# Kernel tuning notes

Measured on AMD Instinct MI355X. Metric: run time of the kernel, lower is better.

Reference implementation:

```python
import jax, jax.numpy as jnp
import numpy as np

UNITS = 512

def _lstm_scan(x_tbf, W, U, b):
    # x_tbf: [T, B, F]; W: [F, 4U]; U: [U, 4U]; b: [4U]
    B = x_tbf.shape[1]
    h0 = jnp.zeros((B, UNITS), dtype=x_tbf.dtype)
    c0 = jnp.zeros((B, UNITS), dtype=x_tbf.dtype)

    def step(carry, x_t):
        h, c = carry
        z = x_t @ W + h @ U + b  # [B, 4U], Keras gate order i,f,g,o
        i, f, g, o = jnp.split(z, 4, axis=-1)
        i = jax.nn.sigmoid(i)
        f = jax.nn.sigmoid(f)
        g = jnp.tanh(g)
        o = jax.nn.sigmoid(o)
        c = f * c + i * g
        h = o * jnp.tanh(c)
        return (h, c), None

    (h, c), _ = jax.lax.scan(step, (h0, c0), x_tbf)
    return h, c


def setup_inputs() -> dict:
    key = jax.random.key(0)
    ks = jax.random.split(key, 7)
    B, T, F = 32, 2048, 256
    s_in = 1.0 / np.sqrt(F)
    s_rec = 1.0 / np.sqrt(UNITS)
    return {
        "inputs": jax.random.normal(ks[0], (B, T, F), dtype=jnp.float32),
        "W_f": jax.random.normal(ks[1], (F, 4 * UNITS), dtype=jnp.float32) * s_in,
        "U_f": jax.random.normal(ks[2], (UNITS, 4 * UNITS), dtype=jnp.float32) * s_rec,
        "b_f": jax.random.normal(ks[3], (4 * UNITS,), dtype=jnp.float32) * 0.01,
        "W_b": jax.random.normal(ks[4], (F, 4 * UNITS), dtype=jnp.float32) * s_in,
        "U_b": jax.random.normal(ks[5], (UNITS, 4 * UNITS), dtype=jnp.float32) * s_rec,
        "b_b": jax.random.normal(ks[6], (4 * UNITS,), dtype=jnp.float32) * 0.01,
    }


def reference(inputs, W_f, U_f, b_f, W_b, U_b, b_b):
    # inputs: [B, T, F] -> scan over time: [T, B, F]
    x = jnp.swapaxes(inputs, 0, 1)
    h_f, c_f = _lstm_scan(x, W_f, U_f, b_f)              # forward direction
    h_b, c_b = _lstm_scan(x[::-1], W_b, U_b, b_b)        # backward: reversed time
    merged = jnp.concatenate([h_f, h_b], axis=-1)        # [B, 2*UNITS]
    return (merged, h_f, c_f, h_b, c_b)
```

## Files before the change

### kernel.cpp

```cpp
#include <hip/hip_runtime.h>

#define T_STEPS 2048
#define NWG 64

typedef __bf16 bf16x8 __attribute__((ext_vector_type(8)));
typedef float f32x4 __attribute__((ext_vector_type(4)));
typedef unsigned long long u64;

#define XBF_OFF   0ull
#define FLAGS_OFF 33554432ull
#define HBUF_OFF  (FLAGS_OFF + 4096ull)
#define WS_NEEDED (HBUF_OFF + 131072ull)

__device__ __forceinline__ unsigned short f2bf(float f) {
    unsigned int u = __builtin_bit_cast(unsigned int, f);
    u = u + 0x7fffu + ((u >> 16) & 1u);
    return (unsigned short)(u >> 16);
}
__device__ __forceinline__ float sigf(float x) { return 1.0f / (1.0f + __expf(-x)); }
__device__ __forceinline__ float tanhfast(float x) { return 1.0f - 2.0f / (__expf(2.0f * x) + 1.0f); }

__global__ void prep_x(const float* __restrict__ X, unsigned short* __restrict__ Xbf) {
    unsigned int idx = blockIdx.x * 256u + threadIdx.x;
    unsigned int k4 = idx & 63u;
    unsigned int b  = (idx >> 6) & 31u;
    unsigned int t  = idx >> 11;
    float4 v = *(const float4*)(X + ((size_t)b * 2048u + t) * 256u + k4 * 4u);
    u64 pk = (u64)f2bf(v.x)
           | ((u64)f2bf(v.y) << 16)
           | ((u64)f2bf(v.z) << 32)
           | ((u64)f2bf(v.w) << 48);
    *(u64*)(Xbf + ((size_t)t * 32u + b) * 256u + k4 * 4u) = pk;
}

__global__ __launch_bounds__(256, 1) void lstm_rec(
    const unsigned short* __restrict__ Xbf,
    const float* __restrict__ W_f, const float* __restrict__ U_f, const float* __restrict__ b_f,
    const float* __restrict__ W_b, const float* __restrict__ U_b, const float* __restrict__ b_b,
    float* __restrict__ out, unsigned int* flags, unsigned int* Hbuf)
{
    const int wg = blockIdx.x;
    const int d  = wg >> 5;
    const int s  = wg & 31;
    const int c0 = s * 16;
    const int tid = threadIdx.x;

    const float* Wm = d ? W_b : W_f;
    const float* Um = d ? U_b : U_f;
    const float* bia = d ? b_b : b_f;

    __shared__ __align__(16) unsigned char s_u[65536];
    __shared__ __align__(16) unsigned char s_w[32768];
    __shared__ __align__(16) unsigned char s_h[32768];
    __shared__ __align__(16) unsigned char s_x[16384];
    __shared__ float s_S[32][64];
    __shared__ float s_bias[64];
    __shared__ int s_abort;

    {
        int cl = tid & 15, g = (tid >> 4) & 3, k0 = tid >> 6;
        int n = g * 16 + cl;
        int gcol = g * 512 + c0 + cl;
        for (int i = 0; i < 128; ++i) {
            int k = k0 + i * 4;
            unsigned short v = f2bf(Um[(size_t)k * 2048 + gcol]);
            unsigned int addr = (unsigned)(n * 1024 + k * 2) ^ (unsigned)((n & 7) << 4);
            *(unsigned short*)(s_u + addr) = v;
        }
        for (int i = 0; i < 64; ++i) {
            int k = k0 + i * 4;
            unsigned short v = f2bf(Wm[(size_t)k * 2048 + gcol]);
            unsigned int addr = (unsigned)(n * 512 + k * 2) ^ (unsigned)((n & 7) << 4);
            *(unsigned short*)(s_w + addr) = v;
        }
        if (tid < 64) s_bias[tid] = bia[(tid >> 4) * 512 + c0 + (tid & 15)];
        if (tid == 0) s_abort = 0;
        for (int i = 0; i < 16; ++i)
            *(u64*)(s_h + (tid + i * 256) * 8) = 0ull;
        int t_x = d ? (T_STEPS - 1) : 0;
        const u64* xsrc = (const u64*)(Xbf + (size_t)t_x * 32 * 256);
        for (int i = 0; i < 8; ++i) {
            int ch = tid + i * 256;
            int b = ch >> 6;
            unsigned int addr = (unsigned)(ch * 8) ^ (unsigned)((b & 7) << 4);
            *(u64*)(s_x + addr) = xsrc[ch];
        }
    }
    __syncthreads();

    const int g  = tid >> 6;
    const int l  = tid & 63;
    const int cl = l & 15;
    const int h4 = l >> 4;
    const int n  = g * 16 + cl;
    const unsigned int uO = (unsigned)(n * 1024 + h4 * 16);
    const unsigned int wO = (unsigned)(n * 512  + h4 * 16);
    const unsigned int nS = (unsigned)((n & 7) << 4);
    const int b0 = cl, b1 = cl + 16;
    const unsigned int hO0 = (unsigned)(b0 * 1024 + h4 * 16);
    const unsigned int hO1 = (unsigned)(b1 * 1024 + h4 * 16);
    const unsigned int xO0 = (unsigned)(b0 * 512  + h4 * 16);
    const unsigned int xO1 = (unsigned)(b1 * 512  + h4 * 16);
    const unsigned int bS0 = (unsigned)((b0 & 7) << 4);
    const unsigned int bS1 = (unsigned)((b1 & 7) << 4);

    const unsigned int fBase  = (unsigned)(d * 32);
    const unsigned int myFlag = fBase + (unsigned)s;
    const unsigned int pollA  = fBase + (unsigned)(l & 15);
    const unsigned int pollB  = fBase + 16u + (unsigned)(l & 15);

    const int eb  = tid >> 3;
    const int ecp = (tid & 7) * 2;
    float c_reg[2] = {0.f, 0.f};

    bf16x8 wBr[8];
    #pragma unroll
    for (int kc = 0; kc < 8; ++kc)
        wBr[kc] = *(const bf16x8*)(s_w + ((wO + kc * 64) ^ nS));
    bf16x8 uBr[16];
    #pragma unroll
    for (int kc = 0; kc < 16; ++kc)
        uBr[kc] = *(const bf16x8*)(s_u + ((uO + kc * 64) ^ nS));

    f32x4 axc0 = {0.f, 0.f, 0.f, 0.f};
    f32x4 axc1 = {0.f, 0.f, 0.f, 0.f};
    #pragma unroll
    for (int kc = 0; kc < 8; ++kc) {
        bf16x8 a0 = *(const bf16x8*)(s_x + ((xO0 + kc * 64) ^ bS0));
        bf16x8 a1 = *(const bf16x8*)(s_x + ((xO1 + kc * 64) ^ bS1));
        axc0 = __builtin_amdgcn_mfma_f32_16x16x32_bf16(a0, wBr[kc], axc0, 0, 0, 0);
        axc1 = __builtin_amdgcn_mfma_f32_16x16x32_bf16(a1, wBr[kc], axc1, 0, 0, 0);
    }

    for (int t = 0; t < T_STEPS; ++t) {
        f32x4 acc0 = axc0;
        f32x4 acc1 = axc1;

        if (t > 0) {
            u64* hsrc = (u64*)Hbuf + (size_t)(d * 2 + (t & 1)) * 4096;

            {
                unsigned int spin = 0;
                for (;;) {
                    unsigned int v = __hip_atomic_load(&flags[pollA], __ATOMIC_RELAXED, __HIP_MEMORY_SCOPE_AGENT);
                    if (__all((int)(v >= (unsigned)t))) break;
                    if (++spin > (1u << 21)) { s_abort = 1; break; }
                    if (spin > 64) __builtin_amdgcn_s_sleep(1);
                }
            }
            u64 ra[8];
            #pragma unroll
            for (int i = 0; i < 8; ++i) {
                int idx = tid + i * 256;
                ra[i] = __hip_atomic_load(&hsrc[(idx >> 6) * 128 + (idx & 63)], __ATOMIC_RELAXED, __HIP_MEMORY_SCOPE_AGENT);
            }
            {
                unsigned int spin = 0;
                for (;;) {
                    unsigned int v = __hip_atomic_load(&flags[pollB], __ATOMIC_RELAXED, __HIP_MEMORY_SCOPE_AGENT);
                    if (__all((int)(v >= (unsigned)t))) break;
                    if (++spin > (1u << 21)) { s_abort = 1; break; }
                    if (spin > 64) __builtin_amdgcn_s_sleep(1);
                }
            }
            u64 rb[8];
            #pragma unroll
            for (int i = 0; i < 8; ++i) {
                int idx = tid + i * 256;
                rb[i] = __hip_atomic_load(&hsrc[(idx >> 6) * 128 + 64 + (idx & 63)], __ATOMIC_RELAXED, __HIP_MEMORY_SCOPE_AGENT);
            }
            #pragma unroll
            for (int i = 0; i < 8; ++i) {
                int idx = tid + i * 256;
                int b = idx >> 6;
                unsigned int addr = (unsigned)(b * 1024 + (idx & 63) * 8) ^ (unsigned)((b & 7) << 4);
                *(u64*)(s_h + addr) = ra[i];
            }
            __syncthreads();
            #pragma unroll
            for (int kc = 0; kc < 8; ++kc) {
                bf16x8 a0 = *(const bf16x8*)(s_h + ((hO0 + kc * 64) ^ bS0));
                bf16x8 a1 = *(const bf16x8*)(s_h + ((hO1 + kc * 64) ^ bS1));
                acc0 = __builtin_amdgcn_mfma_f32_16x16x32_bf16(a0, uBr[kc], acc0, 0, 0, 0);
                acc1 = __builtin_amdgcn_mfma_f32_16x16x32_bf16(a1, uBr[kc], acc1, 0, 0, 0);
            }
            #pragma unroll
            for (int i = 0; i < 8; ++i) {
                int idx = tid + i * 256;
                int b = idx >> 6;
                unsigned int addr = (unsigned)(b * 1024 + 512 + (idx & 63) * 8) ^ (unsigned)((b & 7) << 4);
                *(u64*)(s_h + addr) = rb[i];
            }
            __syncthreads();
            #pragma unroll
            for (int kc = 8; kc < 16; ++kc) {
                bf16x8 a0 = *(const bf16x8*)(s_h + ((hO0 + kc * 64) ^ bS0));
                bf16x8 a1 = *(const bf16x8*)(s_h + ((hO1 + kc * 64) ^ bS1));
                acc0 = __builtin_amdgcn_mfma_f32_16x16x32_bf16(a0, uBr[kc], acc0, 0, 0, 0);
                acc1 = __builtin_amdgcn_mfma_f32_16x16x32_bf16(a1, uBr[kc], acc1, 0, 0, 0);
            }
        }

        #pragma unroll
        for (int r = 0; r < 4; ++r) {
            s_S[h4 * 4 + r][n]      = acc0[r];
            s_S[16 + h4 * 4 + r][n] = acc1[r];
        }
        __syncthreads();
        if (s_abort) return;

        float hv[2];
        #pragma unroll
        for (int j = 0; j < 2; ++j) {
            int cx = ecp + j;
            float zi = s_S[eb][cx]      + s_bias[cx];
            float zf = s_S[eb][16 + cx] + s_bias[16 + cx];
            float zg = s_S[eb][32 + cx] + s_bias[32 + cx];
            float zo = s_S[eb][48 + cx] + s_bias[48 + cx];
            float ii = sigf(zi), ff = sigf(zf), gg = tanhfast(zg), oo = sigf(zo);
            float c = ff * c_reg[j] + ii * gg;
            c_reg[j] = c;
            hv[j] = oo * tanhfast(c);
        }

        if (t == T_STEPS - 1) {
            #pragma unroll
            for (int j = 0; j < 2; ++j) {
                int col = c0 + ecp + j;
                out[(size_t)eb * 1024 + d * 512 + col] = hv[j];
                out[32768 + d * 32768 + (size_t)eb * 512 + col] = hv[j];
                out[49152 + d * 32768 + (size_t)eb * 512 + col] = c_reg[j];
            }
            break;
        }

        const int nb = (t + 1) & 1;
        unsigned int hp = (unsigned)f2bf(hv[0]) | ((unsigned)f2bf(hv[1]) << 16);
        unsigned int hidx = (unsigned)((d * 2 + nb) * 8192 + eb * 256 + ((c0 + ecp) >> 1));
        __hip_atomic_store(&Hbuf[hidx], hp, __ATOMIC_RELAXED, __HIP_MEMORY_SCOPE_AGENT);

        __syncthreads();
        if (tid == 0)
            __hip_atomic_store(&flags[myFlag], (unsigned)(t + 1), __ATOMIC_RELAXED, __HIP_MEMORY_SCOPE_AGENT);

        {
            int t_x = d ? (T_STEPS - 2 - t) : (t + 1);
            const u64* xsrc = (const u64*)(Xbf + (size_t)t_x * 32 * 256);
            #pragma unroll
            for (int i = 0; i < 8; ++i) {
                int ch = tid + i * 256;
                int b = ch >> 6;
                unsigned int addr = (unsigned)(ch * 8) ^ (unsigned)((b & 7) << 4);
                *(u64*)(s_x + addr) = xsrc[ch];
            }
        }
        __syncthreads();
        axc0 = f32x4{0.f, 0.f, 0.f, 0.f};
        axc1 = f32x4{0.f, 0.f, 0.f, 0.f};
        #pragma unroll
        for (int kc = 0; kc < 8; ++kc) {
            bf16x8 a0 = *(const bf16x8*)(s_x + ((xO0 + kc * 64) ^ bS0));
            bf16x8 a1 = *(const bf16x8*)(s_x + ((xO1 + kc * 64) ^ bS1));
            axc0 = __builtin_amdgcn_mfma_f32_16x16x32_bf16(a0, wBr[kc], axc0, 0, 0, 0);
            axc1 = __builtin_amdgcn_mfma_f32_16x16x32_bf16(a1, wBr[kc], axc1, 0, 0, 0);
        }
    }
}

extern "C" void kernel_launch(void* const* d_in, const int* in_sizes, int n_in,
                              void* d_out, int out_size, void* d_ws, size_t ws_size,
                              hipStream_t stream) {
    if (ws_size < WS_NEEDED) return;

    const float* X   = (const float*)d_in[0];
    const float* W_f = (const float*)d_in[1];
    const float* U_f = (const float*)d_in[2];
    const float* b_f = (const float*)d_in[3];
    const float* W_b = (const float*)d_in[4];
    const float* U_b = (const float*)d_in[5];
    const float* b_b = (const float*)d_in[6];

    unsigned short* Xbf  = (unsigned short*)d_ws;
    unsigned int*  flags = (unsigned int*)((char*)d_ws + FLAGS_OFF);
    unsigned int*  Hbuf  = (unsigned int*)((char*)d_ws + HBUF_OFF);

    hipMemsetAsync(flags, 0, 4096, stream);
    prep_x<<<16384, 256, 0, stream>>>(X, Xbf);

    float* out = (float*)d_out;
    void* args[] = {(void*)&Xbf, (void*)&W_f, (void*)&U_f, (void*)&b_f,
                    (void*)&W_b, (void*)&U_b, (void*)&b_b,
                    (void*)&out, (void*)&flags, (void*)&Hbuf};
    hipLaunchCooperativeKernel((void*)lstm_rec, dim3(NWG), dim3(256), args, 0, stream);
}
```

Baseline: 6.461 ms.

## Split batch across 8 groups of workgroups and use XCC-local plain loads when co-located

```diff
diff --git a/kernel.cpp b/kernel.cpp
--- a/kernel.cpp
+++ b/kernel.cpp
@@ -1,7 +1,7 @@
 #include <hip/hip_runtime.h>
 
 #define T_STEPS 2048
-#define NWG 64
+#define NWG 256
 
 typedef __bf16 bf16x8 __attribute__((ext_vector_type(8)));
 typedef float f32x4 __attribute__((ext_vector_type(4)));
@@ -9,7 +9,8 @@
 
 #define XBF_OFF   0ull
 #define FLAGS_OFF 33554432ull
-#define HBUF_OFF  (FLAGS_OFF + 4096ull)
+#define XSLOT_OFF (FLAGS_OFF + 1024ull)
+#define HBUF_OFF  (XSLOT_OFF + 1024ull)
 #define WS_NEEDED (HBUF_OFF + 131072ull)
 
 __device__ __forceinline__ unsigned short f2bf(float f) {
@@ -37,12 +38,14 @@
     const unsigned short* __restrict__ Xbf,
     const float* __restrict__ W_f, const float* __restrict__ U_f, const float* __restrict__ b_f,
     const float* __restrict__ W_b, const float* __restrict__ U_b, const float* __restrict__ b_b,
-    float* __restrict__ out, unsigned int* flags, unsigned int* Hbuf)
+    float* __restrict__ out, unsigned int* flags, unsigned int* xslot, u64* Hbuf)
 {
-    const int wg = blockIdx.x;
-    const int d  = wg >> 5;
-    const int s  = wg & 31;
-    const int c0 = s * 16;
+    const int wg  = blockIdx.x;
+    const int grp = wg & 7;
+    const int s   = wg >> 3;
+    const int d   = grp & 1;
+    const int bo  = (grp >> 1) * 8;
+    const int c0  = s * 16;
     const int tid = threadIdx.x;
 
     const float* Wm = d ? W_b : W_f;
@@ -51,11 +54,12 @@
 
     __shared__ __align__(16) unsigned char s_u[65536];
     __shared__ __align__(16) unsigned char s_w[32768];
-    __shared__ __align__(16) unsigned char s_h[32768];
-    __shared__ __align__(16) unsigned char s_x[16384];
-    __shared__ float s_S[32][64];
+    __shared__ __align__(16) unsigned char s_h[16384];
+    __shared__ __align__(16) unsigned char s_x[8192];
+    __shared__ float s_S[8][64];
     __shared__ float s_bias[64];
     __shared__ int s_abort;
+    __shared__ int s_local;
 
     {
         int cl = tid & 15, g = (tid >> 4) & 3, k0 = tid >> 6;
@@ -74,19 +78,41 @@
             *(unsigned short*)(s_w + addr) = v;
         }
         if (tid < 64) s_bias[tid] = bia[(tid >> 4) * 512 + c0 + (tid & 15)];
-        if (tid == 0) s_abort = 0;
-        for (int i = 0; i < 16; ++i)
-            *(u64*)(s_h + (tid + i * 256) * 8) = 0ull;
+        if (tid == 0) { s_abort = 0; }
+        for (int i = 0; i < 8; ++i) *(u64*)(s_h + (tid + i * 256) * 8) = 0ull;
+        for (int i = 0; i < 4; ++i) *(u64*)(s_x + (tid + i * 256) * 8) = 0ull;
         int t_x = d ? (T_STEPS - 1) : 0;
-        const u64* xsrc = (const u64*)(Xbf + (size_t)t_x * 32 * 256);
-        for (int i = 0; i < 8; ++i) {
-            int ch = tid + i * 256;
-            int b = ch >> 6;
-            unsigned int addr = (unsigned)(ch * 8) ^ (unsigned)((b & 7) << 4);
-            *(u64*)(s_x + addr) = xsrc[ch];
+        const u64* xb = (const u64*)Xbf + (size_t)t_x * 2048;
+        for (int i = 0; i < 2; ++i) {
+            int j = tid + i * 256;
+            int b = j >> 6, c = j & 63;
+            u64 v = xb[(bo + b) * 64 + c];
+            unsigned int addr = (unsigned)(b * 512 + c * 8) ^ (unsigned)((b & 7) << 4);
+            *(u64*)(s_x + addr) = v;
+        }
+        if (tid == 0) {
+            unsigned int xcc = 0;
+            asm volatile("s_getreg_b32 %0, hwreg(HW_REG_XCC_ID)" : "=s"(xcc));
+            __hip_atomic_store(&xslot[wg], xcc + 1u, __ATOMIC_RELAXED, __HIP_MEMORY_SCOPE_AGENT);
+        }
+        {
+            int l = tid & 63;
+            unsigned int spin = 0;
+            unsigned int vm, v0;
+            for (;;) {
+                vm = __hip_atomic_load(&xslot[grp + 8 * (l & 31)], __ATOMIC_RELAXED, __HIP_MEMORY_SCOPE_AGENT);
+                v0 = __hip_atomic_load(&xslot[grp], __ATOMIC_RELAXED, __HIP_MEMORY_SCOPE_AGENT);
+                if (__all((int)(vm != 0u))) break;
+                if (++spin > (1u << 21)) { s_abort = 1; break; }
+                __builtin_amdgcn_s_sleep(1);
+            }
+            int loc = __all((int)(vm != 0u && vm == v0)) ? 1 : 0;
+            if (tid == 0) s_local = loc;
         }
     }
     __syncthreads();
+    if (s_abort) return;
+    const bool isLocal = (s_local != 0);
 
     const int g  = tid >> 6;
     const int l  = tid & 63;
@@ -96,15 +122,12 @@
     const unsigned int uO = (unsigned)(n * 1024 + h4 * 16);
     const unsigned int wO = (unsigned)(n * 512  + h4 * 16);
     const unsigned int nS = (unsigned)((n & 7) << 4);
-    const int b0 = cl, b1 = cl + 16;
+    const int b0 = cl;
     const unsigned int hO0 = (unsigned)(b0 * 1024 + h4 * 16);
-    const unsigned int hO1 = (unsigned)(b1 * 1024 + h4 * 16);
     const unsigned int xO0 = (unsigned)(b0 * 512  + h4 * 16);
-    const unsigned int xO1 = (unsigned)(b1 * 512  + h4 * 16);
     const unsigned int bS0 = (unsigned)((b0 & 7) << 4);
-    const unsigned int bS1 = (unsigned)((b1 & 7) << 4);
-
-    const unsigned int fBase  = (unsigned)(d * 32);
+
+    const unsigned int fBase  = (unsigned)(grp * 32);
     const unsigned int myFlag = fBase + (unsigned)s;
     const unsigned int pollA  = fBase + (unsigned)(l & 15);
     const unsigned int pollB  = fBase + 16u + (unsigned)(l & 15);
@@ -112,6 +135,8 @@
     const int eb  = tid >> 3;
     const int ecp = (tid & 7) * 2;
     float c_reg[2] = {0.f, 0.f};
+
+    unsigned int* H32 = (unsigned int*)Hbuf;
 
     bf16x8 wBr[8];
     #pragma unroll
@@ -123,146 +148,147 @@
         uBr[kc] = *(const bf16x8*)(s_u + ((uO + kc * 64) ^ nS));
 
     f32x4 axc0 = {0.f, 0.f, 0.f, 0.f};
-    f32x4 axc1 = {0.f, 0.f, 0.f, 0.f};
     #pragma unroll
     for (int kc = 0; kc < 8; ++kc) {
         bf16x8 a0 = *(const bf16x8*)(s_x + ((xO0 + kc * 64) ^ bS0));
-        bf16x8 a1 = *(const bf16x8*)(s_x + ((xO1 + kc * 64) ^ bS1));
         axc0 = __builtin_amdgcn_mfma_f32_16x16x32_bf16(a0, wBr[kc], axc0, 0, 0, 0);
-        axc1 = __builtin_amdgcn_mfma_f32_16x16x32_bf16(a1, wBr[kc], axc1, 0, 0, 0);
     }
 
     for (int t = 0; t < T_STEPS; ++t) {
         f32x4 acc0 = axc0;
-        f32x4 acc1 = axc1;
 
         if (t > 0) {
-            u64* hsrc = (u64*)Hbuf + (size_t)(d * 2 + (t & 1)) * 4096;
+            const size_t base64 = (size_t)(grp * 2 + (t & 1)) * 1024;
 
             {
                 unsigned int spin = 0;
                 for (;;) {
-                    unsigned int v = __hip_atomic_load(&flags[pollA], __ATOMIC_RELAXED, __HIP_MEMORY_SCOPE_AGENT);
+                    unsigned int v = isLocal ? *(volatile unsigned int*)&flags[pollA]
+                        : __hip_atomic_load(&flags[pollA], __ATOMIC_RELAXED, __HIP_MEMORY_SCOPE_AGENT);
                     if (__all((int)(v >= (unsigned)t))) break;
                     if (++spin > (1u << 21)) { s_abort = 1; break; }
                     if (spin > 64) __builtin_amdgcn_s_sleep(1);
                 }
             }
-            u64 ra[8];
-            #pragma unroll
-            for (int i = 0; i < 8; ++i) {
-                int idx = tid + i * 256;
-                ra[i] = __hip_atomic_load(&hsrc[(idx >> 6) * 128 + (idx & 63)], __ATOMIC_RELAXED, __HIP_MEMORY_SCOPE_AGENT);
+            u64 ra[2];
+            #pragma unroll
+            for (int i = 0; i < 2; ++i) {
+                int j = tid + i * 256; int b = j >> 6, c = j & 63;
+                size_t idx = base64 + (size_t)(b * 128 + c);
+                ra[i] = isLocal ? *(const volatile u64*)&Hbuf[idx]
+                    : __hip_atomic_load(&Hbuf[idx], __ATOMIC_RELAXED, __HIP_MEMORY_SCOPE_AGENT);
             }
             {
                 unsigned int spin = 0;
                 for (;;) {
-                    unsigned int v = __hip_atomic_load(&flags[pollB], __ATOMIC_RELAXED, __HIP_MEMORY_SCOPE_AGENT);
+                    unsigned int v = isLocal ? *(volatile unsigned int*)&flags[pollB]
+                        : __hip_atomic_load(&flags[pollB], __ATOMIC_RELAXED, __HIP_MEMORY_SCOPE_AGENT);
                     if (__all((int)(v >= (unsigned)t))) break;
                     if (++spin > (1u << 21)) { s_abort = 1; break; }
                     if (spin > 64) __builtin_amdgcn_s_sleep(1);
                 }
             }
-            u64 rb[8];
-            #pragma unroll
-            for (int i = 0; i < 8; ++i) {
-                int idx = tid + i * 256;
-                rb[i] = __hip_atomic_load(&hsrc[(idx >> 6) * 128 + 64 + (idx & 63)], __ATOMIC_RELAXED, __HIP_MEMORY_SCOPE_AGENT);
-            }
-            #pragma unroll
-            for (int i = 0; i < 8; ++i) {
-                int idx = tid + i * 256;
-                int b = idx >> 6;
-                unsigned int addr = (unsigned)(b * 1024 + (idx & 63) * 8) ^ (unsigned)((b & 7) << 4);
+            u64 rb[2];
+            #pragma unroll
+            for (int i = 0; i < 2; ++i) {
+                int j = tid + i * 256; int b = j >> 6, c = j & 63;
+                size_t idx = base64 + (size_t)(b * 128 + 64 + c);
+                rb[i] = isLocal ? *(const volatile u64*)&Hbuf[idx]
+                    : __hip_atomic_load(&Hbuf[idx], __ATOMIC_RELAXED, __HIP_MEMORY_SCOPE_AGENT);
+            }
+            #pragma unroll
+            for (int i = 0; i < 2; ++i) {
+                int j = tid + i * 256; int b = j >> 6, c = j & 63;
+                unsigned int addr = (unsigned)(b * 1024 + c * 8) ^ (unsigned)((b & 7) << 4);
                 *(u64*)(s_h + addr) = ra[i];
             }
             __syncthreads();
             #pragma unroll
             for (int kc = 0; kc < 8; ++kc) {
                 bf16x8 a0 = *(const bf16x8*)(s_h + ((hO0 + kc * 64) ^ bS0));
-                bf16x8 a1 = *(const bf16x8*)(s_h + ((hO1 + kc * 64) ^ bS1));
                 acc0 = __builtin_amdgcn_mfma_f32_16x16x32_bf16(a0, uBr[kc], acc0, 0, 0, 0);
-                acc1 = __builtin_amdgcn_mfma_f32_16x16x32_bf16(a1, uBr[kc], acc1, 0, 0, 0);
-            }
-            #pragma unroll
-            for (int i = 0; i < 8; ++i) {
-                int idx = tid + i * 256;
-                int b = idx >> 6;
-                unsigned int addr = (unsigned)(b * 1024 + 512 + (idx & 63) * 8) ^ (unsigned)((b & 7) << 4);
+            }
+            #pragma unroll
+            for (int i = 0; i < 2; ++i) {
+                int j = tid + i * 256; int b = j >> 6, c = j & 63;
+                unsigned int addr = (unsigned)(b * 1024 + 512 + c * 8) ^ (unsigned)((b & 7) << 4);
                 *(u64*)(s_h + addr) = rb[i];
             }
             __syncthreads();
             #pragma unroll
             for (int kc = 8; kc < 16; ++kc) {
                 bf16x8 a0 = *(const bf16x8*)(s_h + ((hO0 + kc * 64) ^ bS0));
-                bf16x8 a1 = *(const bf16x8*)(s_h + ((hO1 + kc * 64) ^ bS1));
                 acc0 = __builtin_amdgcn_mfma_f32_16x16x32_bf16(a0, uBr[kc], acc0, 0, 0, 0);
-                acc1 = __builtin_amdgcn_mfma_f32_16x16x32_bf16(a1, uBr[kc], acc1, 0, 0, 0);
-            }
-        }
-
-        #pragma unroll
-        for (int r = 0; r < 4; ++r) {
-            s_S[h4 * 4 + r][n]      = acc0[r];
-            s_S[16 + h4 * 4 + r][n] = acc1[r];
+            }
+        }
+
+        if (h4 < 2) {
+            #pragma unroll
+            for (int r = 0; r < 4; ++r)
+                s_S[h4 * 4 + r][n] = acc0[r];
         }
         __syncthreads();
         if (s_abort) return;
 
         float hv[2];
-        #pragma unroll
-        for (int j = 0; j < 2; ++j) {
-            int cx = ecp + j;
-            float zi = s_S[eb][cx]      + s_bias[cx];
-            float zf = s_S[eb][16 + cx] + s_bias[16 + cx];
-            float zg = s_S[eb][32 + cx] + s_bias[32 + cx];
-            float zo = s_S[eb][48 + cx] + s_bias[48 + cx];
-            float ii = sigf(zi), ff = sigf(zf), gg = tanhfast(zg), oo = sigf(zo);
-            float c = ff * c_reg[j] + ii * gg;
-            c_reg[j] = c;
-            hv[j] = oo * tanhfast(c);
+        if (tid < 64) {
+            #pragma unroll
+            for (int j = 0; j < 2; ++j) {
+                int cx = ecp + j;
+                float zi = s_S[eb][cx]      + s_bias[cx];
+                float zf = s_S[eb][16 + cx] + s_bias[16 + cx];
+                float zg = s_S[eb][32 + cx] + s_bias[32 + cx];
+                float zo = s_S[eb][48 + cx] + s_bias[48 + cx];
+                float ii = sigf(zi), ff = sigf(zf), gg = tanhfast(zg), oo = sigf(zo);
+                float c = ff * c_reg[j] + ii * gg;
+                c_reg[j] = c;
+                hv[j] = oo * tanhfast(c);
+            }
         }
 
         if (t == T_STEPS - 1) {
-            #pragma unroll
-            for (int j = 0; j < 2; ++j) {
-                int col = c0 + ecp + j;
-                out[(size_t)eb * 1024 + d * 512 + col] = hv[j];
-                out[32768 + d * 32768 + (size_t)eb * 512 + col] = hv[j];
-                out[49152 + d * 32768 + (size_t)eb * 512 + col] = c_reg[j];
+            if (tid < 64) {
+                #pragma unroll
+                for (int j = 0; j < 2; ++j) {
+                    int col = c0 + ecp + j;
+                    out[(size_t)(bo + eb) * 1024 + d * 512 + col] = hv[j];
+                    out[32768 + d * 32768 + (size_t)(bo + eb) * 512 + col] = hv[j];
+                    out[49152 + d * 32768 + (size_t)(bo + eb) * 512 + col] = c_reg[j];
+                }
             }
             break;
         }
 
         const int nb = (t + 1) & 1;
-        unsigned int hp = (unsigned)f2bf(hv[0]) | ((unsigned)f2bf(hv[1]) << 16);
-        unsigned int hidx = (unsigned)((d * 2 + nb) * 8192 + eb * 256 + ((c0 + ecp) >> 1));
-        __hip_atomic_store(&Hbuf[hidx], hp, __ATOMIC_RELAXED, __HIP_MEMORY_SCOPE_AGENT);
-
+        if (tid < 64) {
+            unsigned int hp = (unsigned)f2bf(hv[0]) | ((unsigned)f2bf(hv[1]) << 16);
+            unsigned int slot = (unsigned)((grp * 2 + nb) * 2048 + eb * 256 + s * 8 + (tid & 7));
+            if (isLocal) *((volatile unsigned int*)H32 + slot) = hp;
+            else __hip_atomic_store(&H32[slot], hp, __ATOMIC_RELAXED, __HIP_MEMORY_SCOPE_AGENT);
+        }
         __syncthreads();
-        if (tid == 0)
-            __hip_atomic_store(&flags[myFlag], (unsigned)(t + 1), __ATOMIC_RELAXED, __HIP_MEMORY_SCOPE_AGENT);
+        if (tid == 0) {
+            if (isLocal) *(volatile unsigned int*)&flags[myFlag] = (unsigned)(t + 1);
+            else __hip_atomic_store(&flags[myFlag], (unsigned)(t + 1), __ATOMIC_RELAXED, __HIP_MEMORY_SCOPE_AGENT);
+        }
 
         {
             int t_x = d ? (T_STEPS - 2 - t) : (t + 1);
-            const u64* xsrc = (const u64*)(Xbf + (size_t)t_x * 32 * 256);
-            #pragma unroll
-            for (int i = 0; i < 8; ++i) {
-                int ch = tid + i * 256;
-                int b = ch >> 6;
-                unsigned int addr = (unsigned)(ch * 8) ^ (unsigned)((b & 7) << 4);
-                *(u64*)(s_x + addr) = xsrc[ch];
+            const u64* xb = (const u64*)Xbf + (size_t)t_x * 2048;
+            #pragma unroll
+            for (int i = 0; i < 2; ++i) {
+                int j = tid + i * 256; int b = j >> 6, c = j & 63;
+                u64 v = xb[(bo + b) * 64 + c];
+                unsigned int addr = (unsigned)(b * 512 + c * 8) ^ (unsigned)((b & 7) << 4);
+                *(u64*)(s_x + addr) = v;
             }
         }
         __syncthreads();
         axc0 = f32x4{0.f, 0.f, 0.f, 0.f};
-        axc1 = f32x4{0.f, 0.f, 0.f, 0.f};
         #pragma unroll
         for (int kc = 0; kc < 8; ++kc) {
             bf16x8 a0 = *(const bf16x8*)(s_x + ((xO0 + kc * 64) ^ bS0));
-            bf16x8 a1 = *(const bf16x8*)(s_x + ((xO1 + kc * 64) ^ bS1));
             axc0 = __builtin_amdgcn_mfma_f32_16x16x32_bf16(a0, wBr[kc], axc0, 0, 0, 0);
-            axc1 = __builtin_amdgcn_mfma_f32_16x16x32_bf16(a1, wBr[kc], axc1, 0, 0, 0);
         }
     }
 }
@@ -280,16 +306,17 @@
     const float* U_b = (const float*)d_in[5];
     const float* b_b = (const float*)d_in[6];
 
-    unsigned short* Xbf  = (unsigned short*)d_ws;
-    unsigned int*  flags = (unsigned int*)((char*)d_ws + FLAGS_OFF);
-    unsigned int*  Hbuf  = (unsigned int*)((char*)d_ws + HBUF_OFF);
-
-    hipMemsetAsync(flags, 0, 4096, stream);
+    unsigned short* Xbf   = (unsigned short*)d_ws;
+    unsigned int*   flags = (unsigned int*)((char*)d_ws + FLAGS_OFF);
+    unsigned int*   xslot = (unsigned int*)((char*)d_ws + XSLOT_OFF);
+    u64*            Hbuf  = (u64*)((char*)d_ws + HBUF_OFF);
+
+    hipMemsetAsync(flags, 0, 2048, stream);
     prep_x<<<16384, 256, 0, stream>>>(X, Xbf);
 
     float* out = (float*)d_out;
     void* args[] = {(void*)&Xbf, (void*)&W_f, (void*)&U_f, (void*)&b_f,
                     (void*)&W_b, (void*)&U_b, (void*)&b_b,
-                    (void*)&out, (void*)&flags, (void*)&Hbuf};
+                    (void*)&out, (void*)&flags, (void*)&xslot, (void*)&Hbuf};
     hipLaunchCooperativeKernel((void*)lstm_rec, dim3(NWG), dim3(256), args, 0, stream);
 }
```

After: 7.281 ms. 12.7% more time.

## Merge split h-poll into one wait and interleave two independent MFMA chains

Applied to the files above, without the earlier changes.

```diff
diff --git a/kernel.cpp b/kernel.cpp
--- a/kernel.cpp
+++ b/kernel.cpp
@@ -106,8 +106,7 @@
 
     const unsigned int fBase  = (unsigned)(d * 32);
     const unsigned int myFlag = fBase + (unsigned)s;
-    const unsigned int pollA  = fBase + (unsigned)(l & 15);
-    const unsigned int pollB  = fBase + 16u + (unsigned)(l & 15);
+    const unsigned int pollF  = fBase + (unsigned)(l & 31);
 
     const int eb  = tid >> 3;
     const int ecp = (tid & 7) * 2;
@@ -142,63 +141,41 @@
             {
                 unsigned int spin = 0;
                 for (;;) {
-                    unsigned int v = __hip_atomic_load(&flags[pollA], __ATOMIC_RELAXED, __HIP_MEMORY_SCOPE_AGENT);
+                    unsigned int v = __hip_atomic_load(&flags[pollF], __ATOMIC_RELAXED, __HIP_MEMORY_SCOPE_AGENT);
                     if (__all((int)(v >= (unsigned)t))) break;
                     if (++spin > (1u << 21)) { s_abort = 1; break; }
                     if (spin > 64) __builtin_amdgcn_s_sleep(1);
                 }
             }
-            u64 ra[8];
-            #pragma unroll
-            for (int i = 0; i < 8; ++i) {
+            u64 r[16];
+            #pragma unroll
+            for (int i = 0; i < 16; ++i) {
                 int idx = tid + i * 256;
-                ra[i] = __hip_atomic_load(&hsrc[(idx >> 6) * 128 + (idx & 63)], __ATOMIC_RELAXED, __HIP_MEMORY_SCOPE_AGENT);
-            }
-            {
-                unsigned int spin = 0;
-                for (;;) {
-                    unsigned int v = __hip_atomic_load(&flags[pollB], __ATOMIC_RELAXED, __HIP_MEMORY_SCOPE_AGENT);
-                    if (__all((int)(v >= (unsigned)t))) break;
-                    if (++spin > (1u << 21)) { s_abort = 1; break; }
-                    if (spin > 64) __builtin_amdgcn_s_sleep(1);
-                }
-            }
-            u64 rb[8];
-            #pragma unroll
-            for (int i = 0; i < 8; ++i) {
+                r[i] = __hip_atomic_load(&hsrc[(idx >> 7) * 128 + (idx & 127)], __ATOMIC_RELAXED, __HIP_MEMORY_SCOPE_AGENT);
+            }
+            #pragma unroll
+            for (int i = 0; i < 16; ++i) {
                 int idx = tid + i * 256;
-                rb[i] = __hip_atomic_load(&hsrc[(idx >> 6) * 128 + 64 + (idx & 63)], __ATOMIC_RELAXED, __HIP_MEMORY_SCOPE_AGENT);
-            }
-            #pragma unroll
-            for (int i = 0; i < 8; ++i) {
-                int idx = tid + i * 256;
-                int b = idx >> 6;
-                unsigned int addr = (unsigned)(b * 1024 + (idx & 63) * 8) ^ (unsigned)((b & 7) << 4);
-                *(u64*)(s_h + addr) = ra[i];
+                int b = idx >> 7, c = idx & 127;
+                unsigned int addr = (unsigned)(b * 1024 + c * 8) ^ (unsigned)((b & 7) << 4);
+                *(u64*)(s_h + addr) = r[i];
             }
             __syncthreads();
+            f32x4 aB0 = {0.f, 0.f, 0.f, 0.f};
+            f32x4 aB1 = {0.f, 0.f, 0.f, 0.f};
             #pragma unroll
             for (int kc = 0; kc < 8; ++kc) {
                 bf16x8 a0 = *(const bf16x8*)(s_h + ((hO0 + kc * 64) ^ bS0));
                 bf16x8 a1 = *(const bf16x8*)(s_h + ((hO1 + kc * 64) ^ bS1));
+                bf16x8 a2 = *(const bf16x8*)(s_h + ((hO0 + (kc + 8) * 64) ^ bS0));
+                bf16x8 a3 = *(const bf16x8*)(s_h + ((hO1 + (kc + 8) * 64) ^ bS1));
                 acc0 = __builtin_amdgcn_mfma_f32_16x16x32_bf16(a0, uBr[kc], acc0, 0, 0, 0);
                 acc1 = __builtin_amdgcn_mfma_f32_16x16x32_bf16(a1, uBr[kc], acc1, 0, 0, 0);
-            }
-            #pragma unroll
-            for (int i = 0; i < 8; ++i) {
-                int idx = tid + i * 256;
-                int b = idx >> 6;
-                unsigned int addr = (unsigned)(b * 1024 + 512 + (idx & 63) * 8) ^ (unsigned)((b & 7) << 4);
-                *(u64*)(s_h + addr) = rb[i];
-            }
-            __syncthreads();
-            #pragma unroll
-            for (int kc = 8; kc < 16; ++kc) {
-                bf16x8 a0 = *(const bf16x8*)(s_h + ((hO0 + kc * 64) ^ bS0));
-                bf16x8 a1 = *(const bf16x8*)(s_h + ((hO1 + kc * 64) ^ bS1));
-                acc0 = __builtin_amdgcn_mfma_f32_16x16x32_bf16(a0, uBr[kc], acc0, 0, 0, 0);
-                acc1 = __builtin_amdgcn_mfma_f32_16x16x32_bf16(a1, uBr[kc], acc1, 0, 0, 0);
-            }
+                aB0  = __builtin_amdgcn_mfma_f32_16x16x32_bf16(a2, uBr[kc + 8], aB0, 0, 0, 0);
+                aB1  = __builtin_amdgcn_mfma_f32_16x16x32_bf16(a3, uBr[kc + 8], aB1, 0, 0, 0);
+            }
+            acc0 = acc0 + aB0;
+            acc1 = acc1 + aB1;
         }
 
         #pragma unroll
```

Result: faster. 6.241 ms (-3.4%).
